# Performance work log

Hardware: AMD Instinct MI355X
Metric: run time of the kernel (lower is better)

The kernel has to match this reference:

```python
import jax, jax.numpy as jnp
import numpy as np

# Action space: 3 discrete action types, 8 options each (MultiDiscrete nvec)
ACTION_NUMS = np.array([8, 8, 8])
A_TOTAL = int(ACTION_NUMS.sum())          # 24
START_IDX = np.cumsum([0, *ACTION_NUMS[:-1]])  # [0, 8, 16]
F, N, D = 4096, 64, 256                   # frames, agents(actions per frame), feat_size
HID = 140                                 # fixed in ForwardNet


def setup_inputs() -> dict:
    key = jax.random.key(0)
    ks = jax.random.split(key, 8)
    s = lambda fan_in: 1.0 / np.sqrt(fan_in)
    return {
        "current_feature": jax.random.normal(ks[0], (F, N, D), jnp.float32),
        "next_feature": jax.random.normal(ks[1], (F, N, D), jnp.float32),
        "actions": jax.random.randint(ks[2], (F, 3, N), 0, 8, dtype=jnp.int32),
        "W1": jax.random.normal(ks[3], (D + A_TOTAL, HID), jnp.float32) * s(D + A_TOTAL),
        "b1": jnp.zeros((HID,), jnp.float32),
        "W2": jax.random.normal(ks[4], (HID, D), jnp.float32) * s(HID),
        "b2": jnp.zeros((D,), jnp.float32),
        "Wi": jax.random.normal(ks[5], (2 * D, A_TOTAL), jnp.float32) * s(2 * D),
        "bi": jnp.zeros((A_TOTAL,), jnp.float32),
    }


def actions2onehot(actions):
    # actions: [F, T, N] int. Vectorized replacement for the triple Python loop:
    # each (frame, agent) row gets a 1 at START_IDX[type] + action, per type.
    start = jnp.asarray(START_IDX, actions.dtype)          # [T]
    idx = actions + start[None, :, None]                    # [F, T, N]
    oh = jax.nn.one_hot(idx, A_TOTAL, dtype=jnp.float32)    # [F, T, N, A]
    return oh.sum(axis=1)                                   # [F, N, A] (column ranges disjoint)


def reference(current_feature, next_feature, actions, W1, b1, W2, b2, Wi, bi):
    action_one_hot = actions2onehot(actions)                       # [F, N, 24]
    # Forward dynamics (attn_target != ICM branch)
    fwd_in = jnp.concatenate([current_feature, action_one_hot], axis=2)  # [F, N, 280]
    h = jax.nn.leaky_relu(fwd_in @ W1 + b1, negative_slope=0.1)
    next_feature_pred = h @ W2 + b2                                # [F, N, 256]
    # Inverse dynamics
    inv_in = jnp.concatenate([current_feature, next_feature], axis=2)   # [F, N, 512]
    action_pred = inv_in @ Wi + bi                                 # [F, N, 24] per-type logits concatenated
    return next_feature_pred, action_pred
```

## Files before the change

### kernel.cpp

```cpp
#include <hip/hip_runtime.h>
#include <hip/hip_bf16.h>
#include <stdint.h>


typedef __attribute__((ext_vector_type(8))) short short8;
typedef __attribute__((ext_vector_type(4))) float float4v;

#define MFMA16 __builtin_amdgcn_mfma_f32_16x16x32_bf16

__device__ __align__(16) uint16_t g_wpack[98816];

static __device__ __forceinline__ void gl_lds16(const void* g, void* l) {
    __builtin_amdgcn_global_load_lds(
        (const __attribute__((address_space(1))) unsigned int*)g,
        (__attribute__((address_space(3))) unsigned int*)l, 16, 0, 0);
}

static __device__ __forceinline__ uint16_t f2bf(float f) {
    __hip_bfloat16 h = __float2bfloat16(f);
    return *reinterpret_cast<uint16_t*>(&h);
}

static __device__ __forceinline__ int pk2(float lo, float hi) {
    __hip_bfloat162 b = __float22bfloat162_rn(make_float2(lo, hi));
    int u; __builtin_memcpy(&u, &b, 4); return u;
}

static __device__ __forceinline__ short8 cvt8(float4v x0, float4v x1) {
    union { __hip_bfloat162 b2[4]; short8 s; } u;
    u.b2[0] = __float22bfloat162_rn(make_float2(x0[0], x0[1]));
    u.b2[1] = __float22bfloat162_rn(make_float2(x0[2], x0[3]));
    u.b2[2] = __float22bfloat162_rn(make_float2(x1[0], x1[1]));
    u.b2[3] = __float22bfloat162_rn(make_float2(x1[2], x1[3]));
    return u.s;
}

__global__ __launch_bounds__(256) void pack_weights(
    const float* __restrict__ W1, const float* __restrict__ W2,
    const float* __restrict__ Wi)
{
    int e = blockIdx.x * 256 + threadIdx.x;
    if (e >= 98816) return;
    if (e >= 41472 && e < 82432) {
        int le = e - 41472;
        int i = le & 7, lane = (le >> 3) & 63, frag = le >> 9;
        int kt = frag >> 4, nt = frag & 15;
        int k = kt * 32 + ((i >= 4) ? 16 : 0) + ((lane >> 4) << 2) + (i & 3);
        int n = nt * 16 + (lane & 15);
        float v = (k < 140) ? W2[k * 256 + n] : 0.0f;
        g_wpack[e] = f2bf(v);
        return;
    }
    const float* W; int NT, Kr, Nr, ld, le, base;
    if (e < 41472) { W = W1; NT = 9; Kr = 280; Nr = 140; ld = 140; le = e;         base = 0; }
    else           { W = Wi; NT = 2; Kr = 512; Nr = 24;  ld = 24;  le = e - 82432; base = 82432; }
    int i = le & 7, lane = (le >> 3) & 63, frag = le >> 9;
    int kt = frag / NT, nt = frag - kt * NT;
    int k = kt * 32 + ((lane >> 4) << 3) + i;
    int n = nt * 16 + (lane & 15);
    float v = (k < Kr && n < Nr) ? W[k * ld + n] : 0.0f;
    g_wpack[base + le] = f2bf(v);
}

__global__ __launch_bounds__(256, 2) void icm_main(
    const float* __restrict__ cf, const float* __restrict__ nf,
    const int* __restrict__ act,
    const float* __restrict__ b1, const float* __restrict__ b2,
    const float* __restrict__ bi,
    float* __restrict__ out)
{
    __shared__ char smem[67584];
    char* bufA = smem;
    char* bufB = smem + 33792;

    const int tid  = threadIdx.x;
    const int wave = tid >> 6;
    const int lane = tid & 63;
    const int lhi  = lane >> 4;
    const int llo  = lane & 15;

    const long rowbase = (long)blockIdx.x * 128 + wave * 32;
    const char* gw = (const char*)g_wpack;

    auto stage1 = [&](char* dst, int kt) {
        const char* w1b = gw + kt * 9216;
        const char* wib = gw + 164864 + kt * 2048;
        const int nb = (kt == 8) ? 9216 : 11264;
        #pragma unroll
        for (int k = 0; k < 3; ++k) {
            int b = k * 4096 + wave * 1024;
            if (b < nb) {
                const char* src = (b < 9216) ? (w1b + b) : (wib + (b - 9216));
                gl_lds16(src + lane * 16, dst + b);
            }
        }
    };
    auto stage16 = [&](char* dst, const char* src) {
        #pragma unroll
        for (int k = 0; k < 4; ++k) {
            int b = k * 4096 + wave * 1024;
            gl_lds16(src + b + lane * 16, dst + b);
        }
    };
    auto stage32 = [&](char* dst, const char* src) {
        #pragma unroll
        for (int k = 0; k < 8; ++k) {
            int b = k * 4096 + wave * 1024;
            gl_lds16(src + b + lane * 16, dst + b);
        }
    };

    int i0[2], i1[2], i2[2];
    #pragma unroll
    for (int m = 0; m < 2; ++m) {
        long r = rowbase + m * 16 + llo;
        long f = r >> 6; int n = (int)(r & 63);
        i0[m] = act[(f * 3 + 0) * 64 + n];
        i1[m] = act[(f * 3 + 1) * 64 + n] + 8;
        i2[m] = act[(f * 3 + 2) * 64 + n] + 16;
    }

    const float4v fz = {0.f, 0.f, 0.f, 0.f};
    float4v acc1[2][9];
    float4v acc3[2][2];
    #pragma unroll
    for (int m = 0; m < 2; ++m) {
        #pragma unroll
        for (int n = 0; n < 9; ++n) acc1[m][n] = fz;
        acc3[m][0] = fz; acc3[m][1] = fz;
    }

    const float* cfb[2];
    #pragma unroll
    for (int m = 0; m < 2; ++m)
        cfb[m] = cf + (rowbase + m * 16 + llo) * 256 + lhi * 8;

    float4v pa0[2], pa1[2], pb0[2], pb1[2];

    auto g1 = [&](const char* base, int kt) {
        short8 a[2];
        if (kt & 1) { a[0] = cvt8(pb0[0], pb1[0]); a[1] = cvt8(pb0[1], pb1[1]); }
        else        { a[0] = cvt8(pa0[0], pa1[0]); a[1] = cvt8(pa0[1], pa1[1]); }
        if (kt <= 5) {
            int o = (kt + 2) * 32;
            if (kt & 1) {
                #pragma unroll
                for (int m = 0; m < 2; ++m) {
                    pb0[m] = *(const float4v*)(cfb[m] + o);
                    pb1[m] = *(const float4v*)(cfb[m] + o + 4);
                }
            } else {
                #pragma unroll
                for (int m = 0; m < 2; ++m) {
                    pa0[m] = *(const float4v*)(cfb[m] + o);
                    pa1[m] = *(const float4v*)(cfb[m] + o + 4);
                }
            }
        }
        #pragma unroll
        for (int nt = 0; nt < 9; ++nt) {
            short8 bf = *(const short8*)(base + (nt << 10) + (lane << 4));
            acc1[0][nt] = MFMA16(bf, a[0], acc1[0][nt], 0, 0, 0);
            acc1[1][nt] = MFMA16(bf, a[1], acc1[1][nt], 0, 0, 0);
        }
        #pragma unroll
        for (int nt = 0; nt < 2; ++nt) {
            short8 bf = *(const short8*)(base + ((9 + nt) << 10) + (lane << 4));
            acc3[0][nt] = MFMA16(bf, a[0], acc3[0][nt], 0, 0, 0);
            acc3[1][nt] = MFMA16(bf, a[1], acc3[1][nt], 0, 0, 0);
        }
    };

    stage1(bufA, 0); stage1(bufA + 11264, 1); stage1(bufA + 22528, 2);
    #pragma unroll
    for (int m = 0; m < 2; ++m) {
        pa0[m] = *(const float4v*)(cfb[m]);
        pa1[m] = *(const float4v*)(cfb[m] + 4);
        pb0[m] = *(const float4v*)(cfb[m] + 32);
        pb1[m] = *(const float4v*)(cfb[m] + 36);
    }
    __syncthreads();

    stage1(bufB, 3); stage1(bufB + 11264, 4); stage1(bufB + 22528, 5);
    g1(bufA, 0); g1(bufA + 11264, 1); g1(bufA + 22528, 2);
    __syncthreads();

    stage1(bufA, 6); stage1(bufA + 11264, 7); stage1(bufA + 22528, 8);
    g1(bufB, 3); g1(bufB + 11264, 4); g1(bufB + 22528, 5);
    __syncthreads();

    stage16(bufB, gw + 164864 + 16384);
    g1(bufA, 6); g1(bufA + 11264, 7);
    const float* nfb[2];
    #pragma unroll
    for (int m = 0; m < 2; ++m)
        nfb[m] = nf + (rowbase + m * 16 + llo) * 256 + lhi * 8;
    #pragma unroll
    for (int m = 0; m < 2; ++m) {
        pa0[m] = *(const float4v*)(nfb[m]);
        pa1[m] = *(const float4v*)(nfb[m] + 4);
        pb0[m] = *(const float4v*)(nfb[m] + 32);
        pb1[m] = *(const float4v*)(nfb[m] + 36);
    }
    {
        short8 a[2];
        #pragma unroll
        for (int m = 0; m < 2; ++m) {
            #pragma unroll
            for (int i = 0; i < 8; ++i) {
                int kk = lhi * 8 + i;
                a[m][i] = (kk == i0[m] || kk == i1[m] || kk == i2[m])
                              ? (short)0x3F80 : (short)0;
            }
        }
        const char* base = bufA + 22528;
        #pragma unroll
        for (int nt = 0; nt < 9; ++nt) {
            short8 bf = *(const short8*)(base + (nt << 10) + (lane << 4));
            acc1[0][nt] = MFMA16(bf, a[0], acc1[0][nt], 0, 0, 0);
            acc1[1][nt] = MFMA16(bf, a[1], acc1[1][nt], 0, 0, 0);
        }
    }
    __syncthreads();

    stage32(bufA, gw + 82944);

    short8 hb[2][5];
    #pragma unroll
    for (int kt = 0; kt < 5; ++kt) {
        int cLo = 2 * kt * 16 + lhi * 4;
        int cHi = (2 * kt + 1) * 16 + lhi * 4;
        if (cLo > 136) cLo = 136;
        float4v bLo = *(const float4v*)(b1 + cLo);
        float4v bHi = (kt < 4) ? *(const float4v*)(b1 + cHi) : fz;
        #pragma unroll
        for (int m = 0; m < 2; ++m) {
            union { int d[4]; short8 s; } t;
            float v0 = acc1[m][2 * kt][0] + bLo[0]; v0 = v0 > 0.f ? v0 : 0.1f * v0;
            float v1 = acc1[m][2 * kt][1] + bLo[1]; v1 = v1 > 0.f ? v1 : 0.1f * v1;
            float v2 = acc1[m][2 * kt][2] + bLo[2]; v2 = v2 > 0.f ? v2 : 0.1f * v2;
            float v3 = acc1[m][2 * kt][3] + bLo[3]; v3 = v3 > 0.f ? v3 : 0.1f * v3;
            t.d[0] = pk2(v0, v1);
            t.d[1] = pk2(v2, v3);
            if (kt < 4) {
                float w0 = acc1[m][2 * kt + 1][0] + bHi[0]; w0 = w0 > 0.f ? w0 : 0.1f * w0;
                float w1 = acc1[m][2 * kt + 1][1] + bHi[1]; w1 = w1 > 0.f ? w1 : 0.1f * w1;
                float w2 = acc1[m][2 * kt + 1][2] + bHi[2]; w2 = w2 > 0.f ? w2 : 0.1f * w2;
                float w3 = acc1[m][2 * kt + 1][3] + bHi[3]; w3 = w3 > 0.f ? w3 : 0.1f * w3;
                t.d[2] = pk2(w0, w1);
                t.d[3] = pk2(w2, w3);
            } else { t.d[2] = 0; t.d[3] = 0; }
            hb[m][kt] = t.s;
        }
    }

    #pragma unroll 1
    for (int kt = 0; kt < 8; ++kt) {
        short8 a[2];
        if (kt & 1) { a[0] = cvt8(pb0[0], pb1[0]); a[1] = cvt8(pb0[1], pb1[1]); }
        else        { a[0] = cvt8(pa0[0], pa1[0]); a[1] = cvt8(pa0[1], pa1[1]); }
        if (kt <= 5) {
            int o = (kt + 2) * 32;
            if (kt & 1) {
                #pragma unroll
                for (int m = 0; m < 2; ++m) {
                    pb0[m] = *(const float4v*)(nfb[m] + o);
                    pb1[m] = *(const float4v*)(nfb[m] + o + 4);
                }
            } else {
                #pragma unroll
                for (int m = 0; m < 2; ++m) {
                    pa0[m] = *(const float4v*)(nfb[m] + o);
                    pa1[m] = *(const float4v*)(nfb[m] + o + 4);
                }
            }
        }
        #pragma unroll
        for (int nt = 0; nt < 2; ++nt) {
            int f = 2 * kt + nt;
            short8 bf = *(const short8*)(bufB + (f << 10) + (lane << 4));
            acc3[0][nt] = MFMA16(bf, a[0], acc3[0][nt], 0, 0, 0);
            acc3[1][nt] = MFMA16(bf, a[1], acc3[1][nt], 0, 0, 0);
        }
    }
    float* out2 = out + 67108864L;
    #pragma unroll
    for (int m = 0; m < 2; ++m) {
        #pragma unroll
        for (int nt = 0; nt < 2; ++nt) {
            if (nt == 0 || lhi < 2) {
                float4v biv = *(const float4v*)(bi + nt * 16 + lhi * 4);
                long row = rowbase + m * 16 + llo;
                float4v v = acc3[m][nt];
                v[0] += biv[0]; v[1] += biv[1]; v[2] += biv[2]; v[3] += biv[3];
                *(float4v*)(out2 + row * 24 + nt * 16 + lhi * 4) = v;
            }
        }
    }
    __syncthreads();

    float4v acc2[2][16];
    #pragma unroll
    for (int m = 0; m < 2; ++m)
        #pragma unroll
        for (int n = 0; n < 16; ++n) acc2[m][n] = fz;

    stage32(bufB, gw + 82944 + 32768);
    #pragma unroll
    for (int k = 0; k < 2; ++k) {
        const char* base = bufA + (k << 14);
        #pragma unroll
        for (int n = 0; n < 16; ++n) {
            short8 bf = *(const short8*)(base + (n << 10) + (lane << 4));
            acc2[0][n] = MFMA16(bf, hb[0][k], acc2[0][n], 0, 0, 0);
            acc2[1][n] = MFMA16(bf, hb[1][k], acc2[1][n], 0, 0, 0);
        }
    }
    __syncthreads();

    stage16(bufA, gw + 82944 + 65536);
    #pragma unroll
    for (int k = 0; k < 2; ++k) {
        const char* base = bufB + (k << 14);
        #pragma unroll
        for (int n = 0; n < 16; ++n) {
            short8 bf = *(const short8*)(base + (n << 10) + (lane << 4));
            acc2[0][n] = MFMA16(bf, hb[0][2 + k], acc2[0][n], 0, 0, 0);
            acc2[1][n] = MFMA16(bf, hb[1][2 + k], acc2[1][n], 0, 0, 0);
        }
    }
    __syncthreads();

    #pragma unroll
    for (int n = 0; n < 16; ++n) {
        short8 bf = *(const short8*)(bufA + (n << 10) + (lane << 4));
        acc2[0][n] = MFMA16(bf, hb[0][4], acc2[0][n], 0, 0, 0);
        acc2[1][n] = MFMA16(bf, hb[1][4], acc2[1][n], 0, 0, 0);
    }

    #pragma unroll
    for (int m = 0; m < 2; ++m) {
        #pragma unroll
        for (int n = 0; n < 16; ++n) {
            float4v b2v = *(const float4v*)(b2 + n * 16 + lhi * 4);
            long row = rowbase + m * 16 + llo;
            float4v v = acc2[m][n];
            v[0] += b2v[0]; v[1] += b2v[1]; v[2] += b2v[2]; v[3] += b2v[3];
            *(float4v*)(out + row * 256 + n * 16 + lhi * 4) = v;
        }
    }
}

extern "C" void kernel_launch(void* const* d_in, const int* in_sizes, int n_in,
                              void* d_out, int out_size, void* d_ws, size_t ws_size,
                              hipStream_t stream) {
    const float *cf = nullptr, *nf = nullptr, *W1 = nullptr, *b1 = nullptr;
    const float *W2 = nullptr, *b2 = nullptr, *Wi = nullptr, *bi = nullptr;
    const int *ac = nullptr;
    for (int i = 0; i < n_in; ++i) {
        int s = in_sizes[i];
        const void* p = d_in[i];
        switch (s) {
            case 67108864: if (!cf) cf = (const float*)p; else nf = (const float*)p; break;
            case 786432:   ac = (const int*)p;   break;
            case 39200:    W1 = (const float*)p; break;
            case 140:      b1 = (const float*)p; break;
            case 35840:    W2 = (const float*)p; break;
            case 256:      b2 = (const float*)p; break;
            case 12288:    Wi = (const float*)p; break;
            case 24:       bi = (const float*)p; break;
            default: break;
        }
    }
    float* ob = (float*)d_out;

    pack_weights<<<386, 256, 0, stream>>>(W1, W2, Wi);
    icm_main<<<2048, 256, 0, stream>>>(cf, nf, ac, b1, b2, bi, ob);
}
```

Measured before the change: 203.9 us.

## Use 8 waves of 16 rows per block instead of 4 waves of 32 rows

```diff
diff --git a/kernel.cpp b/kernel.cpp
--- a/kernel.cpp
+++ b/kernel.cpp
@@ -62,7 +62,7 @@
     g_wpack[base + le] = f2bf(v);
 }
 
-__global__ __launch_bounds__(256, 2) void icm_main(
+__global__ __launch_bounds__(512, 4) void icm_main(
     const float* __restrict__ cf, const float* __restrict__ nf,
     const int* __restrict__ act,
     const float* __restrict__ b1, const float* __restrict__ b2,
@@ -79,7 +79,7 @@
     const int lhi  = lane >> 4;
     const int llo  = lane & 15;
 
-    const long rowbase = (long)blockIdx.x * 128 + wave * 32;
+    const long rowbase = (long)blockIdx.x * 128 + wave * 16;
     const char* gw = (const char*)g_wpack;
 
     auto stage1 = [&](char* dst, int kt) {
@@ -87,8 +87,8 @@
         const char* wib = gw + 164864 + kt * 2048;
         const int nb = (kt == 8) ? 9216 : 11264;
         #pragma unroll
-        for (int k = 0; k < 3; ++k) {
-            int b = k * 4096 + wave * 1024;
+        for (int k = 0; k < 2; ++k) {
+            int b = k * 8192 + wave * 1024;
             if (b < nb) {
                 const char* src = (b < 9216) ? (w1b + b) : (wib + (b - 9216));
                 gl_lds16(src + lane * 16, dst + b);
@@ -97,88 +97,61 @@
     };
     auto stage16 = [&](char* dst, const char* src) {
         #pragma unroll
-        for (int k = 0; k < 4; ++k) {
-            int b = k * 4096 + wave * 1024;
+        for (int k = 0; k < 2; ++k) {
+            int b = k * 8192 + wave * 1024;
             gl_lds16(src + b + lane * 16, dst + b);
         }
     };
     auto stage32 = [&](char* dst, const char* src) {
         #pragma unroll
-        for (int k = 0; k < 8; ++k) {
-            int b = k * 4096 + wave * 1024;
+        for (int k = 0; k < 4; ++k) {
+            int b = k * 8192 + wave * 1024;
             gl_lds16(src + b + lane * 16, dst + b);
         }
     };
 
-    int i0[2], i1[2], i2[2];
-    #pragma unroll
-    for (int m = 0; m < 2; ++m) {
-        long r = rowbase + m * 16 + llo;
+    int i0, i1, i2;
+    {
+        long r = rowbase + llo;
         long f = r >> 6; int n = (int)(r & 63);
-        i0[m] = act[(f * 3 + 0) * 64 + n];
-        i1[m] = act[(f * 3 + 1) * 64 + n] + 8;
-        i2[m] = act[(f * 3 + 2) * 64 + n] + 16;
+        i0 = act[(f * 3 + 0) * 64 + n];
+        i1 = act[(f * 3 + 1) * 64 + n] + 8;
+        i2 = act[(f * 3 + 2) * 64 + n] + 16;
     }
 
     const float4v fz = {0.f, 0.f, 0.f, 0.f};
-    float4v acc1[2][9];
-    float4v acc3[2][2];
-    #pragma unroll
-    for (int m = 0; m < 2; ++m) {
-        #pragma unroll
-        for (int n = 0; n < 9; ++n) acc1[m][n] = fz;
-        acc3[m][0] = fz; acc3[m][1] = fz;
-    }
-
-    const float* cfb[2];
-    #pragma unroll
-    for (int m = 0; m < 2; ++m)
-        cfb[m] = cf + (rowbase + m * 16 + llo) * 256 + lhi * 8;
-
-    float4v pa0[2], pa1[2], pb0[2], pb1[2];
+    float4v acc1[9];
+    float4v acc3[2];
+    #pragma unroll
+    for (int n = 0; n < 9; ++n) acc1[n] = fz;
+    acc3[0] = fz; acc3[1] = fz;
+
+    const float* cfb = cf + (rowbase + llo) * 256 + lhi * 8;
+
+    float4v pa0, pa1, pb0, pb1;
 
     auto g1 = [&](const char* base, int kt) {
-        short8 a[2];
-        if (kt & 1) { a[0] = cvt8(pb0[0], pb1[0]); a[1] = cvt8(pb0[1], pb1[1]); }
-        else        { a[0] = cvt8(pa0[0], pa1[0]); a[1] = cvt8(pa0[1], pa1[1]); }
+        short8 a = (kt & 1) ? cvt8(pb0, pb1) : cvt8(pa0, pa1);
         if (kt <= 5) {
             int o = (kt + 2) * 32;
-            if (kt & 1) {
-                #pragma unroll
-                for (int m = 0; m < 2; ++m) {
-                    pb0[m] = *(const float4v*)(cfb[m] + o);
-                    pb1[m] = *(const float4v*)(cfb[m] + o + 4);
-                }
-            } else {
-                #pragma unroll
-                for (int m = 0; m < 2; ++m) {
-                    pa0[m] = *(const float4v*)(cfb[m] + o);
-                    pa1[m] = *(const float4v*)(cfb[m] + o + 4);
-                }
-            }
+            if (kt & 1) { pb0 = *(const float4v*)(cfb + o); pb1 = *(const float4v*)(cfb + o + 4); }
+            else        { pa0 = *(const float4v*)(cfb + o); pa1 = *(const float4v*)(cfb + o + 4); }
         }
         #pragma unroll
         for (int nt = 0; nt < 9; ++nt) {
             short8 bf = *(const short8*)(base + (nt << 10) + (lane << 4));
-            acc1[0][nt] = MFMA16(bf, a[0], acc1[0][nt], 0, 0, 0);
-            acc1[1][nt] = MFMA16(bf, a[1], acc1[1][nt], 0, 0, 0);
+            acc1[nt] = MFMA16(bf, a, acc1[nt], 0, 0, 0);
         }
         #pragma unroll
         for (int nt = 0; nt < 2; ++nt) {
             short8 bf = *(const short8*)(base + ((9 + nt) << 10) + (lane << 4));
-            acc3[0][nt] = MFMA16(bf, a[0], acc3[0][nt], 0, 0, 0);
-            acc3[1][nt] = MFMA16(bf, a[1], acc3[1][nt], 0, 0, 0);
+            acc3[nt] = MFMA16(bf, a, acc3[nt], 0, 0, 0);
         }
     };
 
     stage1(bufA, 0); stage1(bufA + 11264, 1); stage1(bufA + 22528, 2);
-    #pragma unroll
-    for (int m = 0; m < 2; ++m) {
-        pa0[m] = *(const float4v*)(cfb[m]);
-        pa1[m] = *(const float4v*)(cfb[m] + 4);
-        pb0[m] = *(const float4v*)(cfb[m] + 32);
-        pb1[m] = *(const float4v*)(cfb[m] + 36);
-    }
+    pa0 = *(const float4v*)(cfb);      pa1 = *(const float4v*)(cfb + 4);
+    pb0 = *(const float4v*)(cfb + 32); pb1 = *(const float4v*)(cfb + 36);
     __syncthreads();
 
     stage1(bufB, 3); stage1(bufB + 11264, 4); stage1(bufB + 22528, 5);
@@ -191,41 +164,28 @@
 
     stage16(bufB, gw + 164864 + 16384);
     g1(bufA, 6); g1(bufA + 11264, 7);
-    const float* nfb[2];
-    #pragma unroll
-    for (int m = 0; m < 2; ++m)
-        nfb[m] = nf + (rowbase + m * 16 + llo) * 256 + lhi * 8;
-    #pragma unroll
-    for (int m = 0; m < 2; ++m) {
-        pa0[m] = *(const float4v*)(nfb[m]);
-        pa1[m] = *(const float4v*)(nfb[m] + 4);
-        pb0[m] = *(const float4v*)(nfb[m] + 32);
-        pb1[m] = *(const float4v*)(nfb[m] + 36);
-    }
+    const float* nfb = nf + (rowbase + llo) * 256 + lhi * 8;
+    pa0 = *(const float4v*)(nfb);      pa1 = *(const float4v*)(nfb + 4);
+    pb0 = *(const float4v*)(nfb + 32); pb1 = *(const float4v*)(nfb + 36);
     {
-        short8 a[2];
-        #pragma unroll
-        for (int m = 0; m < 2; ++m) {
-            #pragma unroll
-            for (int i = 0; i < 8; ++i) {
-                int kk = lhi * 8 + i;
-                a[m][i] = (kk == i0[m] || kk == i1[m] || kk == i2[m])
-                              ? (short)0x3F80 : (short)0;
-            }
+        short8 a;
+        #pragma unroll
+        for (int i = 0; i < 8; ++i) {
+            int kk = lhi * 8 + i;
+            a[i] = (kk == i0 || kk == i1 || kk == i2) ? (short)0x3F80 : (short)0;
         }
         const char* base = bufA + 22528;
         #pragma unroll
         for (int nt = 0; nt < 9; ++nt) {
             short8 bf = *(const short8*)(base + (nt << 10) + (lane << 4));
-            acc1[0][nt] = MFMA16(bf, a[0], acc1[0][nt], 0, 0, 0);
-            acc1[1][nt] = MFMA16(bf, a[1], acc1[1][nt], 0, 0, 0);
+            acc1[nt] = MFMA16(bf, a, acc1[nt], 0, 0, 0);
         }
     }
     __syncthreads();
 
     stage32(bufA, gw + 82944);
 
-    short8 hb[2][5];
+    short8 hb[5];
     #pragma unroll
     for (int kt = 0; kt < 5; ++kt) {
         int cLo = 2 * kt * 16 + lhi * 4;
@@ -233,77 +193,55 @@
         if (cLo > 136) cLo = 136;
         float4v bLo = *(const float4v*)(b1 + cLo);
         float4v bHi = (kt < 4) ? *(const float4v*)(b1 + cHi) : fz;
-        #pragma unroll
-        for (int m = 0; m < 2; ++m) {
-            union { int d[4]; short8 s; } t;
-            float v0 = acc1[m][2 * kt][0] + bLo[0]; v0 = v0 > 0.f ? v0 : 0.1f * v0;
-            float v1 = acc1[m][2 * kt][1] + bLo[1]; v1 = v1 > 0.f ? v1 : 0.1f * v1;
-            float v2 = acc1[m][2 * kt][2] + bLo[2]; v2 = v2 > 0.f ? v2 : 0.1f * v2;
-            float v3 = acc1[m][2 * kt][3] + bLo[3]; v3 = v3 > 0.f ? v3 : 0.1f * v3;
-            t.d[0] = pk2(v0, v1);
-            t.d[1] = pk2(v2, v3);
-            if (kt < 4) {
-                float w0 = acc1[m][2 * kt + 1][0] + bHi[0]; w0 = w0 > 0.f ? w0 : 0.1f * w0;
-                float w1 = acc1[m][2 * kt + 1][1] + bHi[1]; w1 = w1 > 0.f ? w1 : 0.1f * w1;
-                float w2 = acc1[m][2 * kt + 1][2] + bHi[2]; w2 = w2 > 0.f ? w2 : 0.1f * w2;
-                float w3 = acc1[m][2 * kt + 1][3] + bHi[3]; w3 = w3 > 0.f ? w3 : 0.1f * w3;
-                t.d[2] = pk2(w0, w1);
-                t.d[3] = pk2(w2, w3);
-            } else { t.d[2] = 0; t.d[3] = 0; }
-            hb[m][kt] = t.s;
-        }
+        union { int d[4]; short8 s; } t;
+        float v0 = acc1[2 * kt][0] + bLo[0]; v0 = v0 > 0.f ? v0 : 0.1f * v0;
+        float v1 = acc1[2 * kt][1] + bLo[1]; v1 = v1 > 0.f ? v1 : 0.1f * v1;
+        float v2 = acc1[2 * kt][2] + bLo[2]; v2 = v2 > 0.f ? v2 : 0.1f * v2;
+        float v3 = acc1[2 * kt][3] + bLo[3]; v3 = v3 > 0.f ? v3 : 0.1f * v3;
+        t.d[0] = pk2(v0, v1);
+        t.d[1] = pk2(v2, v3);
+        if (kt < 4) {
+            float w0 = acc1[2 * kt + 1][0] + bHi[0]; w0 = w0 > 0.f ? w0 : 0.1f * w0;
+            float w1 = acc1[2 * kt + 1][1] + bHi[1]; w1 = w1 > 0.f ? w1 : 0.1f * w1;
+            float w2 = acc1[2 * kt + 1][2] + bHi[2]; w2 = w2 > 0.f ? w2 : 0.1f * w2;
+            float w3 = acc1[2 * kt + 1][3] + bHi[3]; w3 = w3 > 0.f ? w3 : 0.1f * w3;
+            t.d[2] = pk2(w0, w1);
+            t.d[3] = pk2(w2, w3);
+        } else { t.d[2] = 0; t.d[3] = 0; }
+        hb[kt] = t.s;
     }
 
     #pragma unroll 1
     for (int kt = 0; kt < 8; ++kt) {
-        short8 a[2];
-        if (kt & 1) { a[0] = cvt8(pb0[0], pb1[0]); a[1] = cvt8(pb0[1], pb1[1]); }
-        else        { a[0] = cvt8(pa0[0], pa1[0]); a[1] = cvt8(pa0[1], pa1[1]); }
+        short8 a = (kt & 1) ? cvt8(pb0, pb1) : cvt8(pa0, pa1);
         if (kt <= 5) {
             int o = (kt + 2) * 32;
-            if (kt & 1) {
-                #pragma unroll
-                for (int m = 0; m < 2; ++m) {
-                    pb0[m] = *(const float4v*)(nfb[m] + o);
-                    pb1[m] = *(const float4v*)(nfb[m] + o + 4);
-                }
-            } else {
-                #pragma unroll
-                for (int m = 0; m < 2; ++m) {
-                    pa0[m] = *(const float4v*)(nfb[m] + o);
-                    pa1[m] = *(const float4v*)(nfb[m] + o + 4);
-                }
-            }
+            if (kt & 1) { pb0 = *(const float4v*)(nfb + o); pb1 = *(const float4v*)(nfb + o + 4); }
+            else        { pa0 = *(const float4v*)(nfb + o); pa1 = *(const float4v*)(nfb + o + 4); }
         }
         #pragma unroll
         for (int nt = 0; nt < 2; ++nt) {
             int f = 2 * kt + nt;
             short8 bf = *(const short8*)(bufB + (f << 10) + (lane << 4));
-            acc3[0][nt] = MFMA16(bf, a[0], acc3[0][nt], 0, 0, 0);
-            acc3[1][nt] = MFMA16(bf, a[1], acc3[1][nt], 0, 0, 0);
+            acc3[nt] = MFMA16(bf, a, acc3[nt], 0, 0, 0);
         }
     }
     float* out2 = out + 67108864L;
     #pragma unroll
-    for (int m = 0; m < 2; ++m) {
-        #pragma unroll
-        for (int nt = 0; nt < 2; ++nt) {
-            if (nt == 0 || lhi < 2) {
-                float4v biv = *(const float4v*)(bi + nt * 16 + lhi * 4);
-                long row = rowbase + m * 16 + llo;
-                float4v v = acc3[m][nt];
-                v[0] += biv[0]; v[1] += biv[1]; v[2] += biv[2]; v[3] += biv[3];
-                *(float4v*)(out2 + row * 24 + nt * 16 + lhi * 4) = v;
-            }
-        }
-    }
-    __syncthreads();
-
-    float4v acc2[2][16];
-    #pragma unroll
-    for (int m = 0; m < 2; ++m)
-        #pragma unroll
-        for (int n = 0; n < 16; ++n) acc2[m][n] = fz;
+    for (int nt = 0; nt < 2; ++nt) {
+        if (nt == 0 || lhi < 2) {
+            float4v biv = *(const float4v*)(bi + nt * 16 + lhi * 4);
+            long row = rowbase + llo;
+            float4v v = acc3[nt];
+            v[0] += biv[0]; v[1] += biv[1]; v[2] += biv[2]; v[3] += biv[3];
+            *(float4v*)(out2 + row * 24 + nt * 16 + lhi * 4) = v;
+        }
+    }
+    __syncthreads();
+
+    float4v acc2[16];
+    #pragma unroll
+    for (int n = 0; n < 16; ++n) acc2[n] = fz;
 
     stage32(bufB, gw + 82944 + 32768);
     #pragma unroll
@@ -312,8 +250,7 @@
         #pragma unroll
         for (int n = 0; n < 16; ++n) {
             short8 bf = *(const short8*)(base + (n << 10) + (lane << 4));
-            acc2[0][n] = MFMA16(bf, hb[0][k], acc2[0][n], 0, 0, 0);
-            acc2[1][n] = MFMA16(bf, hb[1][k], acc2[1][n], 0, 0, 0);
+            acc2[n] = MFMA16(bf, hb[k], acc2[n], 0, 0, 0);
         }
     }
     __syncthreads();
@@ -325,8 +262,7 @@
         #pragma unroll
         for (int n = 0; n < 16; ++n) {
             short8 bf = *(const short8*)(base + (n << 10) + (lane << 4));
-            acc2[0][n] = MFMA16(bf, hb[0][2 + k], acc2[0][n], 0, 0, 0);
-            acc2[1][n] = MFMA16(bf, hb[1][2 + k], acc2[1][n], 0, 0, 0);
+            acc2[n] = MFMA16(bf, hb[2 + k], acc2[n], 0, 0, 0);
         }
     }
     __syncthreads();
@@ -334,20 +270,16 @@
     #pragma unroll
     for (int n = 0; n < 16; ++n) {
         short8 bf = *(const short8*)(bufA + (n << 10) + (lane << 4));
-        acc2[0][n] = MFMA16(bf, hb[0][4], acc2[0][n], 0, 0, 0);
-        acc2[1][n] = MFMA16(bf, hb[1][4], acc2[1][n], 0, 0, 0);
-    }
-
-    #pragma unroll
-    for (int m = 0; m < 2; ++m) {
-        #pragma unroll
-        for (int n = 0; n < 16; ++n) {
-            float4v b2v = *(const float4v*)(b2 + n * 16 + lhi * 4);
-            long row = rowbase + m * 16 + llo;
-            float4v v = acc2[m][n];
-            v[0] += b2v[0]; v[1] += b2v[1]; v[2] += b2v[2]; v[3] += b2v[3];
-            *(float4v*)(out + row * 256 + n * 16 + lhi * 4) = v;
-        }
+        acc2[n] = MFMA16(bf, hb[4], acc2[n], 0, 0, 0);
+    }
+
+    #pragma unroll
+    for (int n = 0; n < 16; ++n) {
+        float4v b2v = *(const float4v*)(b2 + n * 16 + lhi * 4);
+        long row = rowbase + llo;
+        float4v v = acc2[n];
+        v[0] += b2v[0]; v[1] += b2v[1]; v[2] += b2v[2]; v[3] += b2v[3];
+        *(float4v*)(out + row * 256 + n * 16 + lhi * 4) = v;
     }
 }
 
@@ -375,5 +307,5 @@
     float* ob = (float*)d_out;
 
     pack_weights<<<386, 256, 0, stream>>>(W1, W2, Wi);
-    icm_main<<<2048, 256, 0, stream>>>(cf, nf, ac, b1, b2, bi, ob);
-}
+    icm_main<<<2048, 512, 0, stream>>>(cf, nf, ac, b1, b2, bi, ob);
+}
```

Measured after the change: 212.9 us. +4.4%, slower.
